# Optimization experiments

Hardware: AMD Instinct MI355X
Metric: run time of the kernel (lower is better)

## Reference

```python
import jax, jax.numpy as jnp
import numpy as np

B, N, C = 2, 4096, 768
H = 12  # num_heads; head_dim = C // H = 64


def setup_inputs() -> dict:
    key = jax.random.key(0)
    kx, kq, kk, kv = jax.random.split(key, 4)
    s = C ** -0.5  # keep param magnitudes sane
    return {
        "x": jax.random.normal(kx, (B, N, C), dtype=jnp.float32),
        "Wq": jax.random.normal(kq, (C, C), dtype=jnp.float32) * s,
        "Wk": jax.random.normal(kk, (C, C), dtype=jnp.float32) * s,
        "Wv": jax.random.normal(kv, (C, C), dtype=jnp.float32) * s,  # created but UNUSED, as in original
    }


def reference(x, Wq, Wk, Wv):
    b, n, c = x.shape
    hd = c // H
    # torch nn.Linear: y = x @ W.T
    q = (x @ Wq.T).reshape(b, n, H, hd).transpose(0, 2, 1, 3)  # [B,H,N,hd]
    k = (x @ Wk.T).reshape(b, n, H, hd).transpose(0, 2, 1, 3)
    # BUG preserved from source: value path uses the K projection, Wv is unused
    v = (x @ Wk.T).reshape(b, n, H, hd).transpose(0, 2, 1, 3)
    # scale by full C (not head_dim), as in source
    attn = jnp.einsum("bhqd,bhkd->bhqk", q, k) * (c ** -0.5)
    attn = jax.nn.softmax(attn, axis=-1)
    out = jnp.einsum("bhqk,bhkd->bhqd", attn, v)  # [B,H,N,hd]
    return out.transpose(0, 2, 1, 3).reshape(b, n, c)
```

## Files before the change

kernel.cpp:

```cpp
#include <hip/hip_runtime.h>

typedef __bf16 bf16;
typedef __bf16 bf16x4 __attribute__((ext_vector_type(4)));
typedef __bf16 bf16x8 __attribute__((ext_vector_type(8)));
typedef float  f32x4  __attribute__((ext_vector_type(4)));
typedef int    int4v  __attribute__((ext_vector_type(4)));

#define NTOK 4096
#define NH   12
#define HD   64
#define CDIM 768

#define K2SCALE 0.05205928442089389f

__device__ __forceinline__ bf16* swz(bf16* base, int row, int byteoff) {
  return (bf16*)((char*)base + row * 128 +
                 ((((byteoff >> 4) ^ (row & 7)) << 4) | (byteoff & 15)));
}
__device__ __forceinline__ const bf16* swz(const bf16* base, int row, int byteoff) {
  return (const bf16*)((const char*)base + row * 128 +
                 ((((byteoff >> 4) ^ (row & 7)) << 4) | (byteoff & 15)));
}

__global__ __launch_bounds__(256) void cast_kernel(
    const float* __restrict__ x, const float* __restrict__ wq, const float* __restrict__ wk,
    bf16* __restrict__ xb, bf16* __restrict__ wqb, bf16* __restrict__ wkb,
    long nx, long nw) {
  long i4 = ((long)blockIdx.x * 256 + threadIdx.x) * 4;
  if (i4 >= nx + 2 * nw) return;
  const float* src; bf16* dst;
  if (i4 < nx)            { src = x  + i4;            dst = xb  + i4; }
  else if (i4 < nx + nw)  { src = wq + (i4 - nx);     dst = wqb + (i4 - nx); }
  else                    { src = wk + (i4 - nx - nw); dst = wkb + (i4 - nx - nw); }
  f32x4 v = *(const f32x4*)src;
  *(bf16x4*)dst = __builtin_convertvector(v, bf16x4);
}

__global__ __launch_bounds__(256) void proj_kernel(
    const bf16* __restrict__ xb, const bf16* __restrict__ wqb, const bf16* __restrict__ wkb,
    bf16* __restrict__ Qb, bf16* __restrict__ Kb) {
  __shared__ __align__(16) bf16 Ap[128 * 64];
  __shared__ __align__(16) bf16 Bp[128 * 64];
  const int tid = threadIdx.x;
  const int w = tid >> 6, lane = tid & 63, l15 = lane & 15, quad = lane >> 4;
  const int m0 = blockIdx.x * 128;
  const int j0 = blockIdx.y * 128;
  const bf16* W   = blockIdx.z ? wkb : wqb;
  bf16*       Out = blockIdx.z ? Kb  : Qb;
  const float oscale = blockIdx.z ? 1.0f : K2SCALE;

  const int srow = tid >> 3, scb = (tid & 7) * 16, soff = (tid & 7) * 8;
  const bf16* pa = xb + (long)(m0 + srow) * CDIM + soff;
  const bf16* pb = W  + (long)(j0 + srow) * CDIM + soff;

  f32x4 acc[2][8] = {};
  int4v rA[4], rB[4];
#pragma unroll
  for (int i = 0; i < 4; ++i) {
    rA[i] = *(const int4v*)(pa + (long)i * 32 * CDIM);
    rB[i] = *(const int4v*)(pb + (long)i * 32 * CDIM);
  }

  for (int kt = 0; kt < CDIM / 64; ++kt) {
    __syncthreads();
#pragma unroll
    for (int i = 0; i < 4; ++i) {
      *(int4v*)swz(Ap, srow + i * 32, scb) = rA[i];
      *(int4v*)swz(Bp, srow + i * 32, scb) = rB[i];
    }
    __syncthreads();
    const long koff = (long)((kt == CDIM / 64 - 1) ? kt : kt + 1) * 64;
#pragma unroll
    for (int i = 0; i < 4; ++i) {
      rA[i] = *(const int4v*)(pa + (long)i * 32 * CDIM + koff);
      rB[i] = *(const int4v*)(pb + (long)i * 32 * CDIM + koff);
    }
#pragma unroll
    for (int kk = 0; kk < 2; ++kk) {
      bf16x8 a[2], b[8];
#pragma unroll
      for (int rt = 0; rt < 2; ++rt)
        a[rt] = *(const bf16x8*)swz(Ap, w * 32 + rt * 16 + l15, kk * 64 + quad * 16);
#pragma unroll
      for (int ct = 0; ct < 8; ++ct)
        b[ct] = *(const bf16x8*)swz(Bp, ct * 16 + l15, kk * 64 + quad * 16);
#pragma unroll
      for (int rt = 0; rt < 2; ++rt)
#pragma unroll
        for (int ct = 0; ct < 8; ++ct)
          acc[rt][ct] = __builtin_amdgcn_mfma_f32_16x16x32_bf16(a[rt], b[ct], acc[rt][ct], 0, 0, 0);
    }
  }
#pragma unroll
  for (int rt = 0; rt < 2; ++rt)
#pragma unroll
    for (int ct = 0; ct < 8; ++ct)
#pragma unroll
      for (int reg = 0; reg < 4; ++reg) {
        int m = m0 + w * 32 + rt * 16 + quad * 4 + reg;
        int j = j0 + ct * 16 + l15;
        int b = m >> 12, n = m & (NTOK - 1);
        int h = j >> 6, d = j & (HD - 1);
        Out[(((long)(b * NH + h) * NTOK + n) << 6) + d] = (bf16)(acc[rt][ct][reg] * oscale);
      }
}

__global__ __launch_bounds__(256) void transpose_kernel(
    const bf16* __restrict__ Kb, bf16* __restrict__ Ktb) {
  __shared__ __align__(16) bf16 T[64 * 72];
  const int tid = threadIdx.x;
  const int n0 = blockIdx.x * 64;
  const long bh = blockIdx.y;
#pragma unroll
  for (int i = 0; i < 2; ++i) {
    int c = tid + i * 256;
    int row = c >> 3, off = (c & 7) * 8;
    bf16x8 v = *(const bf16x8*)(Kb + ((bh << 12) + n0 + row) * HD + off);
#pragma unroll
    for (int e = 0; e < 8; ++e) T[(off + e) * 72 + row] = v[e];
  }
  __syncthreads();
#pragma unroll
  for (int i = 0; i < 2; ++i) {
    int c = tid + i * 256;
    int d = c >> 3, koff = (c & 7) * 8;
    int4v v = *(const int4v*)(&T[d * 72 + koff]);
    *(int4v*)(Ktb + ((bh << 6) + d) * (long)NTOK + n0 + koff) = v;
  }
}

__global__ __launch_bounds__(256) void attn_kernel(
    const bf16* __restrict__ Qb, const bf16* __restrict__ Kb, const bf16* __restrict__ Ktb,
    float* __restrict__ out) {
  __shared__ __align__(16) bf16 QP[128 * 64];
  __shared__ __align__(16) bf16 Ks[64 * 64];
  __shared__ __align__(16) bf16 Kts[64 * 64];

  const int tid = threadIdx.x;
  const int w = tid >> 6, lane = tid & 63, l15 = lane & 15, quad = lane >> 4;
  const int q0 = blockIdx.x * 128;
  const int bh = blockIdx.y;
  const int b = bh / NH, h = bh % NH;
  const bf16* Qhead  = Qb  + (long)bh * NTOK * HD;
  const bf16* Khead  = Kb  + (long)bh * NTOK * HD;
  const bf16* Kthead = Ktb + (long)bh * HD * NTOK;

  const int srow = tid >> 3, scb = (tid & 7) * 16, soff = (tid & 7) * 8;
  const bf16* pk  = Khead  + (long)srow * HD + soff;
  const bf16* pkt = Kthead + (long)srow * NTOK + soff;

#pragma unroll
  for (int i = 0; i < 4; ++i) {
    int c = tid + i * 256;
    int row = c >> 3, cb = (c & 7) * 16;
    int4v v = *(const int4v*)(Qhead + (long)(q0 + row) * HD + (c & 7) * 8);
    *(int4v*)swz(QP, row, cb) = v;
  }

  int4v rK[2], rKt[2];
#pragma unroll
  for (int i = 0; i < 2; ++i) {
    rK[i]  = *(const int4v*)(pk  + (long)i * 32 * HD);
    rKt[i] = *(const int4v*)(pkt + (long)i * 32 * NTOK);
  }

  __syncthreads();
  bf16x8 bq[2][2];
#pragma unroll
  for (int nt = 0; nt < 2; ++nt)
#pragma unroll
    for (int kk = 0; kk < 2; ++kk)
      bq[nt][kk] = *(const bf16x8*)swz(QP, w * 32 + nt * 16 + l15, kk * 64 + quad * 16);

  f32x4 o[4][2] = {};
  float lacc[2] = {0.f, 0.f};

  for (int kt = 0; kt < NTOK / 64; ++kt) {
    __syncthreads();
#pragma unroll
    for (int i = 0; i < 2; ++i) {
      *(int4v*)swz(Ks,  srow + i * 32, scb) = rK[i];
      *(int4v*)swz(Kts, srow + i * 32, scb) = rKt[i];
    }
    __syncthreads();

    const long knext = (long)((kt == NTOK / 64 - 1) ? kt : kt + 1) * 64;
#pragma unroll
    for (int i = 0; i < 2; ++i) {
      rK[i]  = *(const int4v*)(pk  + knext * HD + (long)i * 32 * HD);
      rKt[i] = *(const int4v*)(pkt + knext + (long)i * 32 * NTOK);
    }

    f32x4 s[4][2] = {};
#pragma unroll
    for (int kk = 0; kk < 2; ++kk) {
      bf16x8 ak[4];
#pragma unroll
      for (int mt = 0; mt < 4; ++mt)
        ak[mt] = *(const bf16x8*)swz(Ks, mt * 16 + l15, kk * 64 + quad * 16);
#pragma unroll
      for (int mt = 0; mt < 4; ++mt)
#pragma unroll
        for (int nt = 0; nt < 2; ++nt)
          s[mt][nt] = __builtin_amdgcn_mfma_f32_16x16x32_bf16(ak[mt], bq[nt][kk], s[mt][nt], 0, 0, 0);
    }

#pragma unroll
    for (int mt = 0; mt < 4; ++mt)
#pragma unroll
      for (int nt = 0; nt < 2; ++nt) {
        f32x4 p;
#pragma unroll
        for (int reg = 0; reg < 4; ++reg) p[reg] = __builtin_amdgcn_exp2f(s[mt][nt][reg]);
        lacc[nt] += (p[0] + p[1]) + (p[2] + p[3]);
        *(bf16x4*)swz(QP, w * 32 + nt * 16 + l15, mt * 32 + quad * 8) =
            __builtin_convertvector(p, bf16x4);
      }

#pragma unroll
    for (int kk = 0; kk < 2; ++kk) {
      bf16x8 av[4], bp[2];
#pragma unroll
      for (int mt = 0; mt < 4; ++mt)
        av[mt] = *(const bf16x8*)swz(Kts, mt * 16 + l15, kk * 64 + quad * 16);
#pragma unroll
      for (int nt = 0; nt < 2; ++nt)
        bp[nt] = *(const bf16x8*)swz(QP, w * 32 + nt * 16 + l15, kk * 64 + quad * 16);
#pragma unroll
      for (int mt = 0; mt < 4; ++mt)
#pragma unroll
        for (int nt = 0; nt < 2; ++nt)
          o[mt][nt] = __builtin_amdgcn_mfma_f32_16x16x32_bf16(av[mt], bp[nt], o[mt][nt], 0, 0, 0);
    }
  }

#pragma unroll
  for (int nt = 0; nt < 2; ++nt) {
    float l = lacc[nt];
    l += __shfl_xor(l, 16, 64);
    l += __shfl_xor(l, 32, 64);
    float rl = 1.0f / l;
    int n = q0 + w * 32 + nt * 16 + l15;
#pragma unroll
    for (int mt = 0; mt < 4; ++mt) {
      f32x4 v;
#pragma unroll
      for (int reg = 0; reg < 4; ++reg) v[reg] = o[mt][nt][reg] * rl;
      *(f32x4*)(&out[((long)(b * NTOK + n)) * CDIM + h * HD + mt * 16 + quad * 4]) = v;
    }
  }
}

extern "C" void kernel_launch(void* const* d_in, const int* in_sizes, int n_in,
                              void* d_out, int out_size, void* d_ws, size_t ws_size,
                              hipStream_t stream) {
  const float* x  = (const float*)d_in[0];
  const float* Wq = (const float*)d_in[1];
  const float* Wk = (const float*)d_in[2];
  float* out = (float*)d_out;
  char* ws = (char*)d_ws;

  const long NX = (long)2 * NTOK * CDIM;
  const long NW = (long)CDIM * CDIM;

  bf16* xb  = (bf16*)(ws);
  bf16* Ktb = (bf16*)(ws);
  bf16* wqb = (bf16*)(ws + NX * 2);
  bf16* wkb = (bf16*)(ws + NX * 2 + NW * 2);
  bf16* Qb  = (bf16*)(ws + NX * 2 + NW * 4);
  bf16* Kb  = (bf16*)(ws + NX * 2 + NW * 4 + NX * 2);

  long tot4 = (NX + 2 * NW) / 4;
  cast_kernel<<<dim3((tot4 + 255) / 256), 256, 0, stream>>>(x, Wq, Wk, xb, wqb, wkb, NX, NW);
  proj_kernel<<<dim3(8192 / 128, CDIM / 128, 2), 256, 0, stream>>>(xb, wqb, wkb, Qb, Kb);
  transpose_kernel<<<dim3(NTOK / 64, 2 * NH), 256, 0, stream>>>(Kb, Ktb);
  attn_kernel<<<dim3(NTOK / 128, 2 * NH), 256, 0, stream>>>(Qb, Kb, Ktb, out);
}
```

Measured before the change: 237.7 us.

## Use direct global-to-LDS loads with double-buffered K tiles in attention

Replaces register-staged global loads followed by LDS stores with global_load_lds DMA in both the projection and attention kernels. Swizzling moves to the source address so the LDS layout still matches the swizzled reads. The attention kernel now double-buffers the K and K^T tiles, so the next tile is prefetched during compute and one barrier per iteration is dropped; s_setprio is added around the MFMA sections. The projection kernel loses its register prefetch and relies on async loads between two barriers, which may expose latency there. The attention path also depends on the direct-to-LDS loads being complete by the next barrier without an explicit vmcnt wait.

After: 291.8 us. 1.23x slower.

```diff
diff --git a/kernel.cpp b/kernel.cpp
--- a/kernel.cpp
+++ b/kernel.cpp
@@ -20,6 +20,11 @@
 __device__ __forceinline__ const bf16* swz(const bf16* base, int row, int byteoff) {
   return (const bf16*)((const char*)base + row * 128 +
                  ((((byteoff >> 4) ^ (row & 7)) << 4) | (byteoff & 15)));
+}
+
+__device__ __forceinline__ void gld16(void* lds, const void* g) {
+  __builtin_amdgcn_global_load_lds((const __attribute__((address_space(1))) void*)g,
+                                   (__attribute__((address_space(3))) void*)lds, 16, 0, 0);
 }
 
 __global__ __launch_bounds__(256) void cast_kernel(
@@ -49,32 +54,23 @@
   bf16*       Out = blockIdx.z ? Kb  : Qb;
   const float oscale = blockIdx.z ? 1.0f : K2SCALE;
 
-  const int srow = tid >> 3, scb = (tid & 7) * 16, soff = (tid & 7) * 8;
-  const bf16* pa = xb + (long)(m0 + srow) * CDIM + soff;
-  const bf16* pb = W  + (long)(j0 + srow) * CDIM + soff;
+  const int srow = tid >> 3;
+  const int sswz = ((tid & 7) ^ (srow & 7)) * 8;
+  const bf16* pa = xb + (long)(m0 + srow) * CDIM + sswz;
+  const bf16* pb = W  + (long)(j0 + srow) * CDIM + sswz;
+  char* da = (char*)Ap + tid * 16;
+  char* db = (char*)Bp + tid * 16;
 
   f32x4 acc[2][8] = {};
-  int4v rA[4], rB[4];
-#pragma unroll
-  for (int i = 0; i < 4; ++i) {
-    rA[i] = *(const int4v*)(pa + (long)i * 32 * CDIM);
-    rB[i] = *(const int4v*)(pb + (long)i * 32 * CDIM);
-  }
 
   for (int kt = 0; kt < CDIM / 64; ++kt) {
     __syncthreads();
 #pragma unroll
     for (int i = 0; i < 4; ++i) {
-      *(int4v*)swz(Ap, srow + i * 32, scb) = rA[i];
-      *(int4v*)swz(Bp, srow + i * 32, scb) = rB[i];
+      gld16(da + i * 4096, pa + (long)kt * 64 + (long)i * 32 * CDIM);
+      gld16(db + i * 4096, pb + (long)kt * 64 + (long)i * 32 * CDIM);
     }
     __syncthreads();
-    const long koff = (long)((kt == CDIM / 64 - 1) ? kt : kt + 1) * 64;
-#pragma unroll
-    for (int i = 0; i < 4; ++i) {
-      rA[i] = *(const int4v*)(pa + (long)i * 32 * CDIM + koff);
-      rB[i] = *(const int4v*)(pb + (long)i * 32 * CDIM + koff);
-    }
 #pragma unroll
     for (int kk = 0; kk < 2; ++kk) {
       bf16x8 a[2], b[8];
@@ -133,8 +129,8 @@
     const bf16* __restrict__ Qb, const bf16* __restrict__ Kb, const bf16* __restrict__ Ktb,
     float* __restrict__ out) {
   __shared__ __align__(16) bf16 QP[128 * 64];
-  __shared__ __align__(16) bf16 Ks[64 * 64];
-  __shared__ __align__(16) bf16 Kts[64 * 64];
+  __shared__ __align__(16) bf16 Ks[2][64 * 64];
+  __shared__ __align__(16) bf16 Kts[2][64 * 64];
 
   const int tid = threadIdx.x;
   const int w = tid >> 6, lane = tid & 63, l15 = lane & 15, quad = lane >> 4;
@@ -145,26 +141,24 @@
   const bf16* Khead  = Kb  + (long)bh * NTOK * HD;
   const bf16* Kthead = Ktb + (long)bh * HD * NTOK;
 
-  const int srow = tid >> 3, scb = (tid & 7) * 16, soff = (tid & 7) * 8;
-  const bf16* pk  = Khead  + (long)srow * HD + soff;
-  const bf16* pkt = Kthead + (long)srow * NTOK + soff;
+  const int srow = tid >> 3;
+  const int sswz = ((tid & 7) ^ (srow & 7)) * 8;
+  const bf16* pk  = Khead  + (long)srow * HD + sswz;
+  const bf16* pkt = Kthead + (long)srow * NTOK + sswz;
 
 #pragma unroll
   for (int i = 0; i < 4; ++i) {
-    int c = tid + i * 256;
-    int row = c >> 3, cb = (c & 7) * 16;
-    int4v v = *(const int4v*)(Qhead + (long)(q0 + row) * HD + (c & 7) * 8);
-    *(int4v*)swz(QP, row, cb) = v;
-  }
-
-  int4v rK[2], rKt[2];
+    int c = tid + i * 256, row = c >> 3;
+    gld16((char*)QP + c * 16,
+          Qhead + (long)(q0 + row) * HD + (((c & 7) ^ (row & 7)) * 8));
+  }
 #pragma unroll
   for (int i = 0; i < 2; ++i) {
-    rK[i]  = *(const int4v*)(pk  + (long)i * 32 * HD);
-    rKt[i] = *(const int4v*)(pkt + (long)i * 32 * NTOK);
-  }
-
+    gld16((char*)Ks[0]  + tid * 16 + i * 4096, pk  + (long)i * 32 * HD);
+    gld16((char*)Kts[0] + tid * 16 + i * 4096, pkt + (long)i * 32 * NTOK);
+  }
   __syncthreads();
+
   bf16x8 bq[2][2];
 #pragma unroll
   for (int nt = 0; nt < 2; ++nt)
@@ -176,34 +170,31 @@
   float lacc[2] = {0.f, 0.f};
 
   for (int kt = 0; kt < NTOK / 64; ++kt) {
-    __syncthreads();
-#pragma unroll
-    for (int i = 0; i < 2; ++i) {
-      *(int4v*)swz(Ks,  srow + i * 32, scb) = rK[i];
-      *(int4v*)swz(Kts, srow + i * 32, scb) = rKt[i];
-    }
-    __syncthreads();
-
-    const long knext = (long)((kt == NTOK / 64 - 1) ? kt : kt + 1) * 64;
-#pragma unroll
-    for (int i = 0; i < 2; ++i) {
-      rK[i]  = *(const int4v*)(pk  + knext * HD + (long)i * 32 * HD);
-      rKt[i] = *(const int4v*)(pkt + knext + (long)i * 32 * NTOK);
+    const int cb = kt & 1;
+    if (kt < NTOK / 64 - 1) {
+      const long ko = (long)(kt + 1) * 64;
+#pragma unroll
+      for (int i = 0; i < 2; ++i) {
+        gld16((char*)Ks[cb ^ 1]  + tid * 16 + i * 4096, pk  + (ko + (long)i * 32) * HD);
+        gld16((char*)Kts[cb ^ 1] + tid * 16 + i * 4096, pkt + ko + (long)i * 32 * NTOK);
+      }
     }
 
     f32x4 s[4][2] = {};
+    __builtin_amdgcn_s_setprio(1);
 #pragma unroll
     for (int kk = 0; kk < 2; ++kk) {
       bf16x8 ak[4];
 #pragma unroll
       for (int mt = 0; mt < 4; ++mt)
-        ak[mt] = *(const bf16x8*)swz(Ks, mt * 16 + l15, kk * 64 + quad * 16);
+        ak[mt] = *(const bf16x8*)swz(Ks[cb], mt * 16 + l15, kk * 64 + quad * 16);
 #pragma unroll
       for (int mt = 0; mt < 4; ++mt)
 #pragma unroll
         for (int nt = 0; nt < 2; ++nt)
           s[mt][nt] = __builtin_amdgcn_mfma_f32_16x16x32_bf16(ak[mt], bq[nt][kk], s[mt][nt], 0, 0, 0);
     }
+    __builtin_amdgcn_s_setprio(0);
 
 #pragma unroll
     for (int mt = 0; mt < 4; ++mt)
@@ -217,12 +208,13 @@
             __builtin_convertvector(p, bf16x4);
       }
 
+    __builtin_amdgcn_s_setprio(1);
 #pragma unroll
     for (int kk = 0; kk < 2; ++kk) {
       bf16x8 av[4], bp[2];
 #pragma unroll
       for (int mt = 0; mt < 4; ++mt)
-        av[mt] = *(const bf16x8*)swz(Kts, mt * 16 + l15, kk * 64 + quad * 16);
+        av[mt] = *(const bf16x8*)swz(Kts[cb], mt * 16 + l15, kk * 64 + quad * 16);
 #pragma unroll
       for (int nt = 0; nt < 2; ++nt)
         bp[nt] = *(const bf16x8*)swz(QP, w * 32 + nt * 16 + l15, kk * 64 + quad * 16);
@@ -232,6 +224,9 @@
         for (int nt = 0; nt < 2; ++nt)
           o[mt][nt] = __builtin_amdgcn_mfma_f32_16x16x32_bf16(av[mt], bp[nt], o[mt][nt], 0, 0, 0);
     }
+    __builtin_amdgcn_s_setprio(0);
+
+    __syncthreads();
   }
 
 #pragma unroll
```

## Load K tiles directly from global into MFMA registers, drop shared staging

Applied to the files above, without the earlier changes.

Removes the shared-memory staging of K and K-transposed tiles, along with both per-iteration barriers. Each wave now loads its MFMA operands straight from global memory (L2/L1 cached). It also adds s_setprio around the MFMA blocks and sets launch bounds to 3 waves per SIMD to raise occupancy. In exchange, the four waves fetch the same K data redundantly from global or cache, and there is no explicit prefetch, so global load latency may be exposed.

Result: slower. 452.6 us (+90.4%).

```diff
diff --git a/kernel.cpp b/kernel.cpp
--- a/kernel.cpp
+++ b/kernel.cpp
@@ -129,12 +129,10 @@
   }
 }
 
-__global__ __launch_bounds__(256) void attn_kernel(
+__global__ __launch_bounds__(256, 3) void attn_kernel(
     const bf16* __restrict__ Qb, const bf16* __restrict__ Kb, const bf16* __restrict__ Ktb,
     float* __restrict__ out) {
   __shared__ __align__(16) bf16 QP[128 * 64];
-  __shared__ __align__(16) bf16 Ks[64 * 64];
-  __shared__ __align__(16) bf16 Kts[64 * 64];
 
   const int tid = threadIdx.x;
   const int w = tid >> 6, lane = tid & 63, l15 = lane & 15, quad = lane >> 4;
@@ -145,10 +143,6 @@
   const bf16* Khead  = Kb  + (long)bh * NTOK * HD;
   const bf16* Kthead = Ktb + (long)bh * HD * NTOK;
 
-  const int srow = tid >> 3, scb = (tid & 7) * 16, soff = (tid & 7) * 8;
-  const bf16* pk  = Khead  + (long)srow * HD + soff;
-  const bf16* pkt = Kthead + (long)srow * NTOK + soff;
-
 #pragma unroll
   for (int i = 0; i < 4; ++i) {
     int c = tid + i * 256;
@@ -156,15 +150,8 @@
     int4v v = *(const int4v*)(Qhead + (long)(q0 + row) * HD + (c & 7) * 8);
     *(int4v*)swz(QP, row, cb) = v;
   }
-
-  int4v rK[2], rKt[2];
-#pragma unroll
-  for (int i = 0; i < 2; ++i) {
-    rK[i]  = *(const int4v*)(pk  + (long)i * 32 * HD);
-    rKt[i] = *(const int4v*)(pkt + (long)i * 32 * NTOK);
-  }
-
   __syncthreads();
+
   bf16x8 bq[2][2];
 #pragma unroll
   for (int nt = 0; nt < 2; ++nt)
@@ -172,38 +159,40 @@
     for (int kk = 0; kk < 2; ++kk)
       bq[nt][kk] = *(const bf16x8*)swz(QP, w * 32 + nt * 16 + l15, kk * 64 + quad * 16);
 
+  const bf16* pK  = Khead  + l15 * HD + quad * 8;
+  const bf16* pKt = Kthead + (long)l15 * NTOK + quad * 8;
+
   f32x4 o[4][2] = {};
   float lacc[2] = {0.f, 0.f};
 
   for (int kt = 0; kt < NTOK / 64; ++kt) {
-    __syncthreads();
-#pragma unroll
-    for (int i = 0; i < 2; ++i) {
-      *(int4v*)swz(Ks,  srow + i * 32, scb) = rK[i];
-      *(int4v*)swz(Kts, srow + i * 32, scb) = rKt[i];
-    }
-    __syncthreads();
-
-    const long knext = (long)((kt == NTOK / 64 - 1) ? kt : kt + 1) * 64;
-#pragma unroll
-    for (int i = 0; i < 2; ++i) {
-      rK[i]  = *(const int4v*)(pk  + knext * HD + (long)i * 32 * HD);
-      rKt[i] = *(const int4v*)(pkt + knext + (long)i * 32 * NTOK);
-    }
+    const bf16* tK  = pK  + (long)kt * 64 * HD;
+    const bf16* tKt = pKt + (long)kt * 64;
+
+    bf16x8 ak[4][2];
+#pragma unroll
+    for (int mt = 0; mt < 4; ++mt)
+#pragma unroll
+      for (int kk = 0; kk < 2; ++kk)
+        ak[mt][kk] = *(const bf16x8*)(tK + mt * 16 * HD + kk * 32);
 
     f32x4 s[4][2] = {};
-#pragma unroll
-    for (int kk = 0; kk < 2; ++kk) {
-      bf16x8 ak[4];
+    __builtin_amdgcn_s_setprio(1);
+#pragma unroll
+    for (int kk = 0; kk < 2; ++kk)
 #pragma unroll
       for (int mt = 0; mt < 4; ++mt)
-        ak[mt] = *(const bf16x8*)swz(Ks, mt * 16 + l15, kk * 64 + quad * 16);
-#pragma unroll
-      for (int mt = 0; mt < 4; ++mt)
 #pragma unroll
         for (int nt = 0; nt < 2; ++nt)
-          s[mt][nt] = __builtin_amdgcn_mfma_f32_16x16x32_bf16(ak[mt], bq[nt][kk], s[mt][nt], 0, 0, 0);
-    }
+          s[mt][nt] = __builtin_amdgcn_mfma_f32_16x16x32_bf16(ak[mt][kk], bq[nt][kk], s[mt][nt], 0, 0, 0);
+    __builtin_amdgcn_s_setprio(0);
+
+    bf16x8 av[4][2];
+#pragma unroll
+    for (int mt = 0; mt < 4; ++mt)
+#pragma unroll
+      for (int kk = 0; kk < 2; ++kk)
+        av[mt][kk] = *(const bf16x8*)(tKt + (long)mt * 16 * NTOK + kk * 32);
 
 #pragma unroll
     for (int mt = 0; mt < 4; ++mt)
@@ -217,12 +206,10 @@
             __builtin_convertvector(p, bf16x4);
       }
 
+    __builtin_amdgcn_s_setprio(1);
 #pragma unroll
     for (int kk = 0; kk < 2; ++kk) {
-      bf16x8 av[4], bp[2];
-#pragma unroll
-      for (int mt = 0; mt < 4; ++mt)
-        av[mt] = *(const bf16x8*)swz(Kts, mt * 16 + l15, kk * 64 + quad * 16);
+      bf16x8 bp[2];
 #pragma unroll
       for (int nt = 0; nt < 2; ++nt)
         bp[nt] = *(const bf16x8*)swz(QP, w * 32 + nt * 16 + l15, kk * 64 + quad * 16);
@@ -230,8 +217,9 @@
       for (int mt = 0; mt < 4; ++mt)
 #pragma unroll
         for (int nt = 0; nt < 2; ++nt)
-          o[mt][nt] = __builtin_amdgcn_mfma_f32_16x16x32_bf16(av[mt], bp[nt], o[mt][nt], 0, 0, 0);
-    }
+          o[mt][nt] = __builtin_amdgcn_mfma_f32_16x16x32_bf16(av[mt][kk], bp[nt], o[mt][nt], 0, 0, 0);
+    }
+    __builtin_amdgcn_s_setprio(0);
   }
 
 #pragma unroll
```
